# Performance work log

Measured on AMD Instinct MI355X. Metric: run time of the kernel, lower is better.

Reference implementation:

```python
import jax, jax.numpy as jnp
import numpy as np
from jax.scipy.special import erf

# ---- problem constants (mirror module __init__ / placedb) ----
NUM_NODES = 2_000_000
NUM_FLOPS = 800_000
XL, YL, XH, YH = 0.0, 0.0, 168.0, 480.0
SX, SY = 1.0, 1.0                 # inst_stddev_x/y; bin pitch == stddev
INV_SX, INV_SY = 1.0 / SX, 1.0 / SY
TRUNC = 2.5
EXT = max(round(TRUNC - 0.5), 0)  # = 2 -> 5x5 smear window
NBX, NBY, NCK, NCE = 168, 480, 8, 8
CAP = 16                          # SLICE_CAPACITY (UltraScale: 16 FF/slice)
INST_AREA = SX * SY               # kernel receives inst_stddev_x*inst_stddev_y
INV_SQRT2 = 1.0 / np.sqrt(2.0)


def setup_inputs() -> dict:
    key = jax.random.key(0)
    k1, k2, k3, k4, k5 = jax.random.split(key, 5)
    x = jax.random.uniform(k1, (NUM_NODES,), minval=XL, maxval=XH, dtype=jnp.float32)
    y = jax.random.uniform(k2, (NUM_NODES,), minval=YL, maxval=YH, dtype=jnp.float32)
    pos = jnp.concatenate([x, y])  # [2*num_nodes]: x block then y block
    node_size_x = jax.random.uniform(k3, (NUM_NODES,), minval=0.1, maxval=1.0, dtype=jnp.float32)
    node_size_y = jax.random.uniform(k4, (NUM_NODES,), minval=0.1, maxval=1.0, dtype=jnp.float32)
    flop_indices = (jnp.arange(NUM_FLOPS, dtype=jnp.int32) * 2)  # unique, in-range
    flop_ctrlSets = jax.random.randint(k5, (NUM_FLOPS, 2), 0, NCK, dtype=jnp.int32)  # (ck, ce)
    return {"pos": pos, "node_size_x": node_size_x, "node_size_y": node_size_y,
            "flop_indices": flop_indices, "flop_ctrlSets": flop_ctrlSets}


def _smear_1d(centers, bin0, nbins, lo_edge, stddev, inv_std):
    """Gaussian integral over each bin in the truncated window. -> bins [F,W], dem [F,W]."""
    offs = jnp.arange(-EXT, EXT + 1, dtype=jnp.int32)
    b = bin0[:, None] + offs[None, :]
    valid = (b >= 0) & (b < nbins)
    bc = jnp.clip(b, 0, nbins - 1)
    lo = lo_edge + bc.astype(centers.dtype) * stddev
    s = inv_std * INV_SQRT2
    dem = 0.5 * (erf((lo + stddev - centers[:, None]) * s) - erf((lo - centers[:, None]) * s))
    return bc, jnp.where(valid, dem, jnp.zeros_like(dem))


def reference(pos, node_size_x, node_size_y, flop_indices, flop_ctrlSets):
    fi = flop_indices.astype(jnp.int32)
    ck = flop_ctrlSets[:, 0].astype(jnp.int32)
    ce = flop_ctrlSets[:, 1].astype(jnp.int32)

    # instance centers
    cx = pos[fi] + 0.5 * node_size_x[fi]
    cy = pos[NUM_NODES + fi] + 0.5 * node_size_y[fi]

    bx0 = jnp.clip(jnp.floor((cx - XL) * INV_SX).astype(jnp.int32), 0, NBX - 1)
    by0 = jnp.clip(jnp.floor((cy - YL) * INV_SY).astype(jnp.int32), 0, NBY - 1)

    bx, demx = _smear_1d(cx, bx0, NBX, XL, SX, INV_SX)  # [F, 5]
    by, demy = _smear_1d(cy, by0, NBY, YL, SY, INV_SY)  # [F, 5]

    # Gaussian-smeared demand contributions [F, 5, 5]
    dem = (INST_AREA * demx[:, :, None] * demy[:, None, :]).astype(pos.dtype)
    # flattened 4D bin index (x, y, ck, ce)
    idx = ((bx[:, :, None] * NBY + by[:, None, :]) * NCK + ck[:, None, None]) * NCE + ce[:, None, None]

    dem_map = jnp.zeros(NBX * NBY * NCK * NCE, dtype=pos.dtype)
    dem_map = dem_map.at[idx.reshape(-1)].add(dem.reshape(-1))
    dem_map = dem_map.reshape(NBX, NBY, NCK, NCE)

    # HALF ctrl mode slice quantization (UltraScale): quarter=CAP/4 FFs share CE,
    # half = 2 quarters share CK/SR, slice = 2 halves.
    quarters = jnp.sum(jnp.ceil(dem_map / (CAP // 4)), axis=3)   # [x,y,ck]
    halves = jnp.sum(jnp.ceil(0.5 * quarters), axis=2)          # [x,y]
    slices = jnp.ceil(0.5 * halves)                             # [x,y]

    tot = dem_map.sum(axis=(2, 3))                              # [x,y]
    scale = jnp.where(tot > 0, slices * CAP / jnp.maximum(tot, 1e-12), jnp.zeros_like(tot))

    # gather quantized area back at each flop's center bin
    areas = INST_AREA * scale[bx0, by0]
    resource_areas = jnp.zeros(NUM_NODES, dtype=pos.dtype).at[fi].set(areas)
    return resource_areas / CAP
```

## Files before the change

### kernel.cpp

```cpp
#include <hip/hip_runtime.h>
#include <math.h>

#define NUM_NODES 2000000
#define NUM_FLOPS 800000
#define NBX 168
#define NBY 480
#define NCK 8
#define NCE 8
#define NBINS (NBX * NBY)
#define YB_ROWS 10
#define NYB 48
#define NBUCK (NYB * NBX)
#define CAPB 210
#define W 2
#define TROWS (YB_ROWS + 8)
#define TILE_F (TROWS * W * 64)
#define S_INVSQRT2 0.7071067811865476f
#define FILL_THREADS (784 * 1024)


struct Rec12 { float cx, cy; int keby; };

__device__ __forceinline__ float fast_erf(float x) {
    float ax = fabsf(x);
    float t = __builtin_amdgcn_rcpf(fmaf(0.3275911f, ax, 1.0f));
    float p = t * fmaf(t, fmaf(t, fmaf(t, fmaf(t, 1.061405429f, -1.453152027f),
                                       1.421413741f), -0.284496736f), 0.254829592f);
    float r = fmaf(-p, __expf(-ax * ax), 1.0f);
    return copysignf(r, x);
}

__global__ void __launch_bounds__(1024)
ff_fill(const float* __restrict__ pos,
        const float* __restrict__ nsx,
        const float* __restrict__ nsy,
        const int* __restrict__ fi,
        const int* __restrict__ cs,
        int* __restrict__ cnt,
        Rec12* __restrict__ rec,
        float* __restrict__ out) {
    __shared__ int h[NBUCK];
    __shared__ int base[NBUCK];
    int tid = threadIdx.x;
    int f = blockIdx.x * blockDim.x + tid;

    for (int g = f; g < NUM_NODES; g += FILL_THREADS) out[g] = 0.f;

    for (int j = tid; j < NBUCK; j += 1024) h[j] = 0;
    __syncthreads();

    bool valid = (f < NUM_FLOPS);
    int b1 = 0, b2 = -1, r1 = 0, r2 = 0, keby = 0;
    float cx = 0.f, cy = 0.f;
    if (valid) {
        int i = fi[f];
        cx = pos[i] + 0.5f * nsx[i];
        cy = pos[NUM_NODES + i] + 0.5f * nsy[i];
        int bx0 = (int)floorf(cx); bx0 = bx0 < 0 ? 0 : (bx0 > NBX - 1 ? NBX - 1 : bx0);
        int by0 = (int)floorf(cy); by0 = by0 < 0 ? 0 : (by0 > NBY - 1 ? NBY - 1 : by0);
        int2 cc = ((const int2*)cs)[f];
        keby = (by0 << 6) | (cc.x * NCE + cc.y);
        int yb = by0 / YB_ROWS;
        int rlo = by0 - yb * YB_ROWS;
        b1 = yb * NBX + bx0;
        r1 = atomicAdd(&h[b1], 1);
        if (rlo <= 1 && yb > 0)                       b2 = b1 - NBX;
        else if (rlo >= YB_ROWS - 2 && yb < NYB - 1)  b2 = b1 + NBX;
        if (b2 >= 0) r2 = atomicAdd(&h[b2], 1);
    }
    __syncthreads();
    for (int j = tid; j < NBUCK; j += 1024)
        base[j] = h[j] ? atomicAdd(&cnt[j], h[j]) : 0;
    __syncthreads();
    if (valid) {
        Rec12 v; v.cx = cx; v.cy = cy; v.keby = keby;
        int s1 = base[b1] + r1;
        if (s1 < CAPB) rec[(size_t)b1 * CAPB + s1] = v;
        if (b2 >= 0) {
            int s2 = base[b2] + r2;
            if (s2 < CAPB) rec[(size_t)b2 * CAPB + s2] = v;
        }
    }
}

__global__ void __launch_bounds__(256, 4)
ff_main(const int* __restrict__ cnt,
        const Rec12* __restrict__ rec,
        float* __restrict__ scale) {
    __shared__ __align__(16) float sh[4 * TILE_F];
    int tid = threadIdx.x;
    int wv = tid >> 6, lane = tid & 63;
    float* wtile = sh + wv * TILE_F;
    int c0 = blockIdx.x * W;
    int yb = blockIdx.y;
    int y0 = yb * YB_ROWS;

    for (int j = tid; j < TILE_F; j += 256)
        ((float4*)sh)[j] = make_float4(0.f, 0.f, 0.f, 0.f);
    __syncthreads();

    int c_lo = c0 - 2 < 0 ? 0 : c0 - 2;
    int c_hi = c0 + W + 1 > NBX - 1 ? NBX - 1 : c0 + W + 1;
    int nb = c_hi - c_lo + 1;
    int start[7];
    start[0] = 0;
#pragma unroll
    for (int k = 0; k < 6; ++k) {
        int n = 0;
        if (k < nb) { n = cnt[yb * NBX + c_lo + k]; n = n < CAPB ? n : CAPB; }
        start[k + 1] = start[k] + n;
    }
    int tot = start[6];
    const Rec12* bb = rec + (size_t)(yb * NBX + c_lo) * CAPB;

    for (int idx = tid; idx < tot; idx += 256) {
        int k = 0, off = idx;
#pragma unroll
        for (int t = 1; t < 6; ++t) { bool g = idx >= start[t]; k = g ? t : k; off = g ? idx - start[t] : off; }
        Rec12 v = bb[(size_t)k * CAPB + off];
        float cx = v.cx, cy = v.cy;
        int ke  = v.keby & 63;
        int by0 = v.keby >> 6;
        int bx0 = c_lo + k;
        float ex[W + 1], ey[6];
#pragma unroll
        for (int i = 0; i <= W; ++i)
            ex[i] = fast_erf(((float)(c0 + i) - cx) * S_INVSQRT2);
#pragma unroll
        for (int j = 0; j < 6; ++j)
            ey[j] = fast_erf(((float)(by0 - 2 + j) - cy) * S_INVSQRT2);
        float dyq[5];
#pragma unroll
        for (int j = 0; j < 5; ++j) dyq[j] = ey[j + 1] - ey[j];
        float dxq[W];
#pragma unroll
        for (int i = 0; i < W; ++i) {
            int col = c0 + i;
            float m = (col >= bx0 - 2 && col <= bx0 + 2) ? 1.f : 0.f;
            dxq[i] = 0.25f * (ex[i + 1] - ex[i]) * m;
        }
        int rr0 = by0 - y0 + 2;

        unsigned long long peers = __ballot(1);
#pragma unroll
        for (int b = 0; b < 6; ++b) {
            unsigned long long bl = __ballot((ke >> b) & 1);
            peers &= ((ke >> b) & 1) ? bl : ~bl;
        }
        int rank = (int)__popcll(peers & ((1ull << lane) - 1ull));

        for (int r = 0;; ++r) {
            if (!__ballot(rank == r)) break;
            if (rank == r) {
                float* t0 = wtile + rr0 * (W * 64) + ke;
                float a0 = t0[0 * 128], a1 = t0[1 * 128], a2 = t0[2 * 128],
                      a3 = t0[3 * 128], a4 = t0[4 * 128];
                float b0 = t0[0 * 128 + 64], b1 = t0[1 * 128 + 64], b2 = t0[2 * 128 + 64],
                      b3 = t0[3 * 128 + 64], b4 = t0[4 * 128 + 64];
                a0 = fmaf(dxq[0], dyq[0], a0); b0 = fmaf(dxq[1], dyq[0], b0);
                a1 = fmaf(dxq[0], dyq[1], a1); b1 = fmaf(dxq[1], dyq[1], b1);
                a2 = fmaf(dxq[0], dyq[2], a2); b2 = fmaf(dxq[1], dyq[2], b2);
                a3 = fmaf(dxq[0], dyq[3], a3); b3 = fmaf(dxq[1], dyq[3], b3);
                a4 = fmaf(dxq[0], dyq[4], a4); b4 = fmaf(dxq[1], dyq[4], b4);
                t0[0 * 128] = a0; t0[1 * 128] = a1; t0[2 * 128] = a2;
                t0[3 * 128] = a3; t0[4 * 128] = a4;
                t0[0 * 128 + 64] = b0; t0[1 * 128 + 64] = b1; t0[2 * 128 + 64] = b2;
                t0[3 * 128 + 64] = b3; t0[4 * 128 + 64] = b4;
            }
            asm volatile("s_waitcnt lgkmcnt(0)" ::: "memory");
        }
    }
    __syncthreads();

    if (tid < YB_ROWS * W) {
        int rl = tid >> 1, cl = tid & 1;
        int off = (rl + 4) * (W * 64) + cl * 64;
        float tot2 = 0.f, halves = 0.f;
#pragma unroll
        for (int ck = 0; ck < NCK; ++ck) {
            float q = 0.f;
#pragma unroll
            for (int h2 = 0; h2 < 2; ++h2) {
                float4 d = make_float4(0.f, 0.f, 0.f, 0.f);
#pragma unroll
                for (int w2 = 0; w2 < 4; ++w2) {
                    float4 e = *(const float4*)(sh + w2 * TILE_F + off + ck * 8 + h2 * 4);
                    d.x += e.x; d.y += e.y; d.z += e.z; d.w += e.w;
                }
                tot2 += d.x + d.y + d.z + d.w;
                q += ceilf(d.x * 0.25f) + ceilf(d.y * 0.25f) +
                     ceilf(d.z * 0.25f) + ceilf(d.w * 0.25f);
            }
            halves += ceilf(0.5f * q);
        }
        float slices = ceilf(0.5f * halves);
        scale[(c0 + cl) * NBY + y0 + rl] = (tot2 > 0.f) ? (slices / fmaxf(tot2, 1e-12f)) : 0.f;
    }
}

__global__ void ff_gather(const float* __restrict__ pos,
                          const float* __restrict__ nsx,
                          const float* __restrict__ nsy,
                          const int* __restrict__ fi,
                          const float* __restrict__ scale,
                          float* __restrict__ out) {
    int f = blockIdx.x * blockDim.x + threadIdx.x;
    if (f >= NUM_FLOPS) return;
    int i = fi[f];
    float cx = pos[i] + 0.5f * nsx[i];
    float cy = pos[NUM_NODES + i] + 0.5f * nsy[i];
    int bx0 = (int)floorf(cx); bx0 = bx0 < 0 ? 0 : (bx0 > NBX - 1 ? NBX - 1 : bx0);
    int by0 = (int)floorf(cy); by0 = by0 < 0 ? 0 : (by0 > NBY - 1 ? NBY - 1 : by0);
    out[i] = scale[bx0 * NBY + by0];
}

extern "C" void kernel_launch(void* const* d_in, const int* in_sizes, int n_in,
                              void* d_out, int out_size, void* d_ws, size_t ws_size,
                              hipStream_t stream) {
    const float* pos = (const float*)d_in[0];
    const float* nsx = (const float*)d_in[1];
    const float* nsy = (const float*)d_in[2];
    const int*   fi  = (const int*)d_in[3];
    const int*   cs  = (const int*)d_in[4];
    float* out = (float*)d_out;

    float* scale = (float*)d_ws;
    int*   cnt   = (int*)(scale + NBINS);
    Rec12* rec   = (Rec12*)(scale + NBINS + NBUCK);

    hipMemsetAsync(cnt, 0, NBUCK * sizeof(int), stream);

    ff_fill<<<784, 1024, 0, stream>>>(pos, nsx, nsy, fi, cs, cnt, rec, out);
    ff_main<<<dim3(NBX / W, NYB), 256, 0, stream>>>(cnt, rec, scale);
    ff_gather<<<(NUM_FLOPS + 255) / 256, 256, 0, stream>>>(pos, nsx, nsy, fi, scale, out);
}
```

Measured before the change: 187.7 us.

## Replace fine-grained bucket scatter with two-level column counting sort

The fill kernel now bins flops by x-column only, stages them in shared memory sorted by column, and writes contiguous runs to global memory. This replaces scattered 12-byte writes into 8064 buckets. A new per-column kernel then sorts each column's records by y-band, including halo duplicates, and publishes bucket start/count tables for the main kernel. The intent is to make the global writes coalesced and cut atomic contention. The cost is an extra kernel launch, a second full pass over the records, and large shared-memory use per block.

```diff
diff --git a/kernel.cpp b/kernel.cpp
--- a/kernel.cpp
+++ b/kernel.cpp
@@ -10,13 +10,15 @@
 #define NBINS (NBX * NBY)
 #define YB_ROWS 10
 #define NYB 48
-#define NBUCK (NYB * NBX)
-#define CAPB 210
+#define CAPC 6720
+#define CAPR 9600
+#define SORT_IT 7
 #define W 2
 #define TROWS (YB_ROWS + 8)
 #define TILE_F (TROWS * W * 64)
 #define S_INVSQRT2 0.7071067811865476f
-#define FILL_THREADS (784 * 1024)
+#define P1_FLOPS 4096
+#define P1_BLOCKS 196
 
 
 struct Rec12 { float cx, cy; int keby; };
@@ -36,55 +38,144 @@
         const float* __restrict__ nsy,
         const int* __restrict__ fi,
         const int* __restrict__ cs,
-        int* __restrict__ cnt,
+        int* __restrict__ colcnt,
         Rec12* __restrict__ rec,
         float* __restrict__ out) {
-    __shared__ int h[NBUCK];
-    __shared__ int base[NBUCK];
+    __shared__ int hist[NBX];
+    __shared__ int ofs[NBX];
+    __shared__ int gbase[NBX];
+    __shared__ int sc[NBX];
+    __shared__ int tot_s;
+    __shared__ Rec12 staged[P1_FLOPS];
     int tid = threadIdx.x;
-    int f = blockIdx.x * blockDim.x + tid;
-
-    for (int g = f; g < NUM_NODES; g += FILL_THREADS) out[g] = 0.f;
-
-    for (int j = tid; j < NBUCK; j += 1024) h[j] = 0;
-    __syncthreads();
-
-    bool valid = (f < NUM_FLOPS);
-    int b1 = 0, b2 = -1, r1 = 0, r2 = 0, keby = 0;
-    float cx = 0.f, cy = 0.f;
-    if (valid) {
-        int i = fi[f];
-        cx = pos[i] + 0.5f * nsx[i];
-        cy = pos[NUM_NODES + i] + 0.5f * nsy[i];
-        int bx0 = (int)floorf(cx); bx0 = bx0 < 0 ? 0 : (bx0 > NBX - 1 ? NBX - 1 : bx0);
-        int by0 = (int)floorf(cy); by0 = by0 < 0 ? 0 : (by0 > NBY - 1 ? NBY - 1 : by0);
-        int2 cc = ((const int2*)cs)[f];
-        keby = (by0 << 6) | (cc.x * NCE + cc.y);
-        int yb = by0 / YB_ROWS;
-        int rlo = by0 - yb * YB_ROWS;
-        b1 = yb * NBX + bx0;
-        r1 = atomicAdd(&h[b1], 1);
-        if (rlo <= 1 && yb > 0)                       b2 = b1 - NBX;
-        else if (rlo >= YB_ROWS - 2 && yb < NYB - 1)  b2 = b1 + NBX;
-        if (b2 >= 0) r2 = atomicAdd(&h[b2], 1);
-    }
-    __syncthreads();
-    for (int j = tid; j < NBUCK; j += 1024)
-        base[j] = h[j] ? atomicAdd(&cnt[j], h[j]) : 0;
-    __syncthreads();
-    if (valid) {
-        Rec12 v; v.cx = cx; v.cy = cy; v.keby = keby;
-        int s1 = base[b1] + r1;
-        if (s1 < CAPB) rec[(size_t)b1 * CAPB + s1] = v;
-        if (b2 >= 0) {
-            int s2 = base[b2] + r2;
-            if (s2 < CAPB) rec[(size_t)b2 * CAPB + s2] = v;
-        }
+    int f0 = blockIdx.x * P1_FLOPS;
+
+    for (int g = blockIdx.x * 1024 + tid; g < NUM_NODES; g += P1_BLOCKS * 1024)
+        out[g] = 0.f;
+
+    for (int j = tid; j < NBX; j += 1024) hist[j] = 0;
+    __syncthreads();
+
+    int colq[4], r1q[4], kebyq[4];
+    float cxq[4], cyq[4];
+    bool vq[4];
+#pragma unroll
+    for (int q = 0; q < 4; ++q) {
+        int f = f0 + q * 1024 + tid;
+        bool valid = f < NUM_FLOPS;
+        vq[q] = valid; colq[q] = 0; r1q[q] = 0; kebyq[q] = 0; cxq[q] = 0.f; cyq[q] = 0.f;
+        if (valid) {
+            int i = fi[f];
+            float cx = pos[i] + 0.5f * nsx[i];
+            float cy = pos[NUM_NODES + i] + 0.5f * nsy[i];
+            int bx0 = (int)floorf(cx); bx0 = bx0 < 0 ? 0 : (bx0 > NBX - 1 ? NBX - 1 : bx0);
+            int by0 = (int)floorf(cy); by0 = by0 < 0 ? 0 : (by0 > NBY - 1 ? NBY - 1 : by0);
+            int2 cc = ((const int2*)cs)[f];
+            int ke = cc.x * NCE + cc.y;
+            colq[q] = bx0; cxq[q] = cx; cyq[q] = cy;
+            kebyq[q] = (bx0 << 15) | (by0 << 6) | ke;
+            r1q[q] = atomicAdd(&hist[bx0], 1);
+        }
+    }
+    __syncthreads();
+    if (tid < NBX) sc[tid] = hist[tid];
+    __syncthreads();
+    for (int d = 1; d < NBX; d <<= 1) {
+        int v2 = 0;
+        if (tid < NBX && tid >= d) v2 = sc[tid - d];
+        __syncthreads();
+        if (tid < NBX) sc[tid] += v2;
+        __syncthreads();
+    }
+    if (tid < NBX) {
+        ofs[tid] = sc[tid] - hist[tid];
+        int nn = hist[tid];
+        gbase[tid] = nn ? atomicAdd(&colcnt[tid], nn) : 0;
+    }
+    if (tid == 0) tot_s = sc[NBX - 1];
+    __syncthreads();
+#pragma unroll
+    for (int q = 0; q < 4; ++q)
+        if (vq[q]) {
+            Rec12 v; v.cx = cxq[q]; v.cy = cyq[q]; v.keby = kebyq[q];
+            staged[ofs[colq[q]] + r1q[q]] = v;
+        }
+    __syncthreads();
+    for (int t = tid; t < tot_s; t += 1024) {
+        Rec12 v = staged[t];
+        int c = (v.keby >> 15) & 255;
+        int slot = gbase[c] + (t - ofs[c]);
+        if (slot < CAPC) rec[(size_t)c * CAPR + slot] = v;
+    }
+}
+
+__global__ void __launch_bounds__(1024)
+ff_sort(const int* __restrict__ colcnt,
+        Rec12* __restrict__ rec,
+        int* __restrict__ bstart,
+        int* __restrict__ bcnt) {
+    __shared__ Rec12 staged[CAPC];
+    __shared__ unsigned short perm[CAPR];
+    __shared__ int hist[NYB];
+    __shared__ int ofs[NYB + 1];
+    int c = blockIdx.x;
+    int tid = threadIdx.x;
+    int n = colcnt[c]; n = n < CAPC ? n : CAPC;
+    Rec12* col = rec + (size_t)c * CAPR;
+    for (int t = tid; t < n; t += 1024) staged[t] = col[t];
+    if (tid < NYB) hist[tid] = 0;
+    __syncthreads();
+
+    int sP[SORT_IT], sH[SORT_IT], ybq[SORT_IT], ybhq[SORT_IT];
+#pragma unroll
+    for (int it = 0; it < SORT_IT; ++it) {
+        int t = it * 1024 + tid;
+        sP[it] = 0; sH[it] = 0; ybq[it] = 0; ybhq[it] = -1;
+        if (t < n) {
+            int by0 = (staged[t].keby >> 6) & 511;
+            int yb = by0 / YB_ROWS;
+            int rlo = by0 - yb * YB_ROWS;
+            ybq[it] = yb;
+            sP[it] = atomicAdd(&hist[yb], 1);
+            int ybh = (rlo <= 1 && yb > 0) ? yb - 1
+                    : ((rlo >= YB_ROWS - 2 && yb < NYB - 1) ? yb + 1 : -1);
+            ybhq[it] = ybh;
+            if (ybh >= 0) sH[it] = atomicAdd(&hist[ybh], 1);
+        }
+    }
+    __syncthreads();
+    if (tid == 0) {
+        int s = 0;
+        for (int g = 0; g < NYB; ++g) { ofs[g] = s; s += hist[g]; }
+        ofs[NYB] = s;
+    }
+    __syncthreads();
+#pragma unroll
+    for (int it = 0; it < SORT_IT; ++it) {
+        int t = it * 1024 + tid;
+        if (t < n) {
+            int ip = ofs[ybq[it]] + sP[it];
+            if (ip < CAPR) perm[ip] = (unsigned short)t;
+            if (ybhq[it] >= 0) {
+                int ih = ofs[ybhq[it]] + sH[it];
+                if (ih < CAPR) perm[ih] = (unsigned short)t;
+            }
+        }
+    }
+    __syncthreads();
+    int m = ofs[NYB]; m = m < CAPR ? m : CAPR;
+    for (int t = tid; t < m; t += 1024) col[t] = staged[perm[t]];
+    if (tid < NYB) {
+        int s0 = ofs[tid];             s0 = s0 < CAPR ? s0 : CAPR;
+        int e0 = ofs[tid] + hist[tid]; e0 = e0 < CAPR ? e0 : CAPR;
+        bstart[c * NYB + tid] = c * CAPR + s0;
+        bcnt[c * NYB + tid]   = e0 - s0;
     }
 }
 
 __global__ void __launch_bounds__(256, 4)
-ff_main(const int* __restrict__ cnt,
+ff_main(const int* __restrict__ bstart,
+        const int* __restrict__ bcnt,
         const Rec12* __restrict__ rec,
         float* __restrict__ scale) {
     __shared__ __align__(16) float sh[4 * TILE_F];
@@ -102,25 +193,31 @@
     int c_lo = c0 - 2 < 0 ? 0 : c0 - 2;
     int c_hi = c0 + W + 1 > NBX - 1 ? NBX - 1 : c0 + W + 1;
     int nb = c_hi - c_lo + 1;
-    int start[7];
+    int start[7], sb6[6];
     start[0] = 0;
 #pragma unroll
     for (int k = 0; k < 6; ++k) {
-        int n = 0;
-        if (k < nb) { n = cnt[yb * NBX + c_lo + k]; n = n < CAPB ? n : CAPB; }
-        start[k + 1] = start[k] + n;
+        int nrec = 0, sbv = 0;
+        if (k < nb) {
+            int b = (c_lo + k) * NYB + yb;
+            nrec = bcnt[b]; sbv = bstart[b];
+        }
+        sb6[k] = sbv;
+        start[k + 1] = start[k] + nrec;
     }
     int tot = start[6];
-    const Rec12* bb = rec + (size_t)(yb * NBX + c_lo) * CAPB;
 
     for (int idx = tid; idx < tot; idx += 256) {
-        int k = 0, off = idx;
-#pragma unroll
-        for (int t = 1; t < 6; ++t) { bool g = idx >= start[t]; k = g ? t : k; off = g ? idx - start[t] : off; }
-        Rec12 v = bb[(size_t)k * CAPB + off];
+        int k = 0, off = idx, base = sb6[0];
+#pragma unroll
+        for (int t = 1; t < 6; ++t) {
+            bool g = idx >= start[t];
+            k = g ? t : k; off = g ? idx - start[t] : off; base = g ? sb6[t] : base;
+        }
+        Rec12 v = rec[(size_t)(base + off)];
         float cx = v.cx, cy = v.cy;
         int ke  = v.keby & 63;
-        int by0 = v.keby >> 6;
+        int by0 = (v.keby >> 6) & 511;
         int bx0 = c_lo + k;
         float ex[W + 1], ey[6];
 #pragma unroll
@@ -136,8 +233,8 @@
 #pragma unroll
         for (int i = 0; i < W; ++i) {
             int col = c0 + i;
-            float m = (col >= bx0 - 2 && col <= bx0 + 2) ? 1.f : 0.f;
-            dxq[i] = 0.25f * (ex[i + 1] - ex[i]) * m;
+            float mm = (col >= bx0 - 2 && col <= bx0 + 2) ? 1.f : 0.f;
+            dxq[i] = 0.25f * (ex[i + 1] - ex[i]) * mm;
         }
         int rr0 = by0 - y0 + 2;
 
@@ -224,13 +321,16 @@
     const int*   cs  = (const int*)d_in[4];
     float* out = (float*)d_out;
 
-    float* scale = (float*)d_ws;
-    int*   cnt   = (int*)(scale + NBINS);
-    Rec12* rec   = (Rec12*)(scale + NBINS + NBUCK);
-
-    hipMemsetAsync(cnt, 0, NBUCK * sizeof(int), stream);
-
-    ff_fill<<<784, 1024, 0, stream>>>(pos, nsx, nsy, fi, cs, cnt, rec, out);
-    ff_main<<<dim3(NBX / W, NYB), 256, 0, stream>>>(cnt, rec, scale);
+    float* scale  = (float*)d_ws;
+    int*   colcnt = (int*)(scale + NBINS);
+    int*   bstart = colcnt + NBX;
+    int*   bcnt   = bstart + NBX * NYB;
+    Rec12* rec    = (Rec12*)(bcnt + NBX * NYB);
+
+    hipMemsetAsync(colcnt, 0, NBX * sizeof(int), stream);
+
+    ff_fill<<<P1_BLOCKS, 1024, 0, stream>>>(pos, nsx, nsy, fi, cs, colcnt, rec, out);
+    ff_sort<<<NBX, 1024, 0, stream>>>(colcnt, rec, bstart, bcnt);
+    ff_main<<<dim3(NBX / W, NYB), 256, 0, stream>>>(bstart, bcnt, rec, scale);
     ff_gather<<<(NUM_FLOPS + 255) / 256, 256, 0, stream>>>(pos, nsx, nsy, fi, scale, out);
 }
```

New measurement: 163.7 us. 1.15x faster.
